# Kernel optimization log

Hardware: AMD Instinct MI355X
Metric: run time of the kernel (lower is better)

The kernel has to match this reference:

```python
import jax, jax.numpy as jnp
import numpy as np

B, T, NE, NH, HD = 4, 1024, 768, 12, 64
CURV = 0.0
EPS = 1e-6
LN_EPS = 1e-5
ROPE_BASE = 10000.0


def project(x, k):
    # Lift Euclidean vector onto Lorentz hyperboloid with curvature K = exp(k):
    # time coord t = sqrt(K + ||x||^2) so that <lx, lx>_L = -K.
    K = jnp.exp(k)
    t = jnp.sqrt(K + jnp.sum(x * x, axis=-1, keepdims=True))
    return jnp.concatenate([t, x], axis=-1)


def lorentz_distance(lq, lk, k):
    # lq, lk: (B, H, T, D+1); k: (1, H, 1, 1) log-curvature.
    # d = sqrt(K) * arccosh(clamp(-<q,k>_L / K, 1+eps))
    K = jnp.exp(k)
    inner = (jnp.einsum('bhid,bhjd->bhij', lq[..., 1:], lk[..., 1:])
             - jnp.einsum('bhi,bhj->bhij', lq[..., 0], lk[..., 0]))
    c = jnp.clip(-inner / K, 1.0 + EPS, None)
    return jnp.sqrt(K) * jnp.arccosh(c)


def lorentz_norm(x):
    # sqrt(|<x,x>_L|) with <x,x>_L = -x0^2 + ||xs||^2  (keepdim)
    inner = -x[..., 0:1] ** 2 + jnp.sum(x[..., 1:] ** 2, axis=-1, keepdims=True)
    return jnp.sqrt(jnp.clip(-inner, EPS, None))


def rotary_tables():
    inv_freq = 1.0 / (ROPE_BASE ** (np.arange(0, HD, 2, dtype=np.float32) / HD))
    t = np.arange(T, dtype=np.float32)
    freqs = np.outer(t, inv_freq)  # (T, HD/2)
    cos = jnp.asarray(np.cos(freqs))[None, :, None, :]  # (1,T,1,HD/2)
    sin = jnp.asarray(np.sin(freqs))[None, :, None, :]
    return cos, sin


def apply_rotary(x, cos, sin):
    # x: (B, T, H, HD)
    x1, x2 = x[..., : HD // 2], x[..., HD // 2:]
    return jnp.concatenate([x1 * cos + x2 * sin, -x1 * sin + x2 * cos], axis=-1)


def layernorm(y, g, b):
    m = jnp.mean(y, axis=-1, keepdims=True)
    v = jnp.mean((y - m) ** 2, axis=-1, keepdims=True)
    return (y - m) / jnp.sqrt(v + LN_EPS) * g + b


def setup_inputs() -> dict:
    key = jax.random.key(0)
    ks = jax.random.split(key, 8)
    s = 0.02
    return {
        'x': jax.random.normal(ks[0], (B, T, NE), dtype=jnp.float32),
        'block_curvature': jnp.asarray(CURV, dtype=jnp.float32),
        'mlp_curvature': jnp.asarray(CURV, dtype=jnp.float32),
        'attn_curvatures': jnp.ones((1, NH, 1, 1), dtype=jnp.float32) * CURV,
        'qkv_w': jax.random.normal(ks[1], (3 * NE, NE + 1), dtype=jnp.float32) * s,
        'attn_proj_w': jax.random.normal(ks[2], (NE, (HD + 1) * NH), dtype=jnp.float32) * s,
        'attn_proj_b': jnp.zeros((NE,), dtype=jnp.float32),
        'mlp_expand_w': jax.random.normal(ks[3], (4 * NE + 3, NE + 1), dtype=jnp.float32) * s,
        'mlp_expand_b': jnp.zeros((4 * NE + 3,), dtype=jnp.float32),
        'mlp_shrink_w': jax.random.normal(ks[4], (NE, 4 * (NE + 1)), dtype=jnp.float32) * s,
        'mlp_shrink_b': jnp.zeros((NE,), dtype=jnp.float32),
        'ln_g': jnp.ones((NE,), dtype=jnp.float32),
        'ln_b': jnp.zeros((NE,), dtype=jnp.float32),
    }


def reference(x, block_curvature, mlp_curvature, attn_curvatures, qkv_w,
              attn_proj_w, attn_proj_b, mlp_expand_w, mlp_expand_b,
              mlp_shrink_w, mlp_shrink_b, ln_g, ln_b):
    cos, sin = rotary_tables()
    causal_bias = jnp.where(
        jnp.triu(jnp.ones((T, T), dtype=bool), k=1), -jnp.inf, 0.0).astype(jnp.float32)

    def block_norm(lx):
        return project(layernorm(lx[..., 1:], ln_g, ln_b), block_curvature)

    def attn(lx):
        qkv = lx @ qkv_w.T  # (B, T, 3*NE)
        q, k, v = jnp.split(qkv, 3, axis=-1)
        q = apply_rotary(q.reshape(B, T, NH, HD), cos, sin)
        k = apply_rotary(k.reshape(B, T, NH, HD), cos, sin)
        v = v.reshape(B, T, NH, HD)
        lq = project(q.transpose(0, 2, 1, 3), attn_curvatures)  # (B,H,T,HD+1)
        lk = project(k.transpose(0, 2, 1, 3), attn_curvatures)
        lv = project(v.transpose(0, 2, 1, 3), attn_curvatures)
        dis = lorentz_distance(lq, lk, attn_curvatures)  # (B,H,T,T)
        aw = jax.nn.softmax(-dis + causal_bias, axis=-1)
        a = jnp.einsum('bhij,bhjd->bhid', aw, lv)  # (B,H,T,HD+1)
        a = a * jnp.sqrt(jnp.exp(attn_curvatures)) / lorentz_norm(a)
        a = a.transpose(0, 2, 1, 3).reshape(B, T, NH * (HD + 1))
        a = a @ attn_proj_w.T + attn_proj_b
        return project(a, block_curvature)

    def mlp(lx):
        h = lx @ mlp_expand_w.T + mlp_expand_b  # (B,T,4*NE+3)
        h = project(h, mlp_curvature)[..., 1:]  # drop time coord back to 4*NE+3
        h = jax.nn.gelu(h, approximate=False)
        h = project(h, mlp_curvature)  # (B,T,4*(NE+1))
        h = h @ mlp_shrink_w.T + mlp_shrink_b
        return project(h, block_curvature)

    def skip(lx, f_lx):
        return project(lx[..., 1:] + f_lx[..., 1:], block_curvature)

    lx = project(x, block_curvature)  # (B,T,NE+1)
    lx = skip(lx, attn(block_norm(lx)))
    lx = skip(lx, mlp(block_norm(lx)))
    return lx
```

## Files before the change

### kernel.cpp

```cpp
#include <hip/hip_runtime.h>
#include <cmath>

typedef unsigned short ushort_t;
typedef __attribute__((ext_vector_type(8))) short short8;
typedef __attribute__((ext_vector_type(4))) float floatx4;

#define NH    12
#define T     1024
#define ROWS  4096
#define NE    768
#define KPA   800
#define KPB   3104
#define NEXP  3200
#define HEXP  3075

__device__ __forceinline__ ushort_t f2bf(float f) {
  union { float f; unsigned u; } v; v.f = f;
  unsigned r = v.u + 0x7fffu + ((v.u >> 16) & 1u);
  return (ushort_t)(r >> 16);
}
__device__ __forceinline__ float bf2f(ushort_t b) {
  union { unsigned u; float f; } v; v.u = ((unsigned)b) << 16;
  return v.f;
}
__device__ __forceinline__ float blk_reduce_sum(float v, float* sm) {
  #pragma unroll
  for (int o = 32; o > 0; o >>= 1) v += __shfl_xor(v, o, 64);
  int lane = threadIdx.x & 63, w = threadIdx.x >> 6;
  __syncthreads();
  if (lane == 0) sm[w] = v;
  __syncthreads();
  return sm[0] + sm[1] + sm[2] + sm[3];
}
__device__ __forceinline__ float red16_sum(float v) {
  #pragma unroll
  for (int o = 1; o < 16; o <<= 1) v += __shfl_xor(v, o, 64);
  return v;
}
__device__ __forceinline__ float red16_max(float v) {
  #pragma unroll
  for (int o = 1; o < 16; o <<= 1) v = fmaxf(v, __shfl_xor(v, o, 64));
  return v;
}

__global__ void cvt_pad(ushort_t* __restrict__ dst, const float* __restrict__ src,
                        int rows, int srcK, int dstK, int rowsPad) {
  int idx = blockIdx.x * 256 + threadIdx.x;
  int total = rowsPad * dstK;
  if (idx >= total) return;
  int r = idx / dstK, c = idx - r * dstK;
  dst[idx] = (r < rows && c < srcK) ? f2bf(src[(size_t)r * srcK + c]) : (ushort_t)0;
}

__global__ void zero_aout_pad_bf(ushort_t* __restrict__ a) {
  int r = blockIdx.x * 256 + threadIdx.x;
  if (r < ROWS) {
    ushort_t* p = a + (size_t)r * KPA + 780;
    #pragma unroll
    for (int j = 0; j < 20; ++j) p[j] = 0;
  }
}

__global__ __launch_bounds__(256) void ln_project(
    const float* __restrict__ xin, const float* __restrict__ g,
    const float* __restrict__ bb, const float* __restrict__ curv,
    ushort_t* __restrict__ outp) {
  __shared__ float sm[4];
  const int row = blockIdx.x;
  const int tid = threadIdx.x;
  const float* xr = xin + (size_t)row * NE;
  float xv[3];
  float s = 0.f, ss = 0.f;
  #pragma unroll
  for (int i = 0; i < 3; ++i) {
    xv[i] = xr[tid + 256 * i];
    s += xv[i]; ss += xv[i] * xv[i];
  }
  s = blk_reduce_sum(s, sm);
  ss = blk_reduce_sum(ss, sm);
  float mean = s * (1.f / 768.f);
  float var = ss * (1.f / 768.f) - mean * mean;
  float rstd = rsqrtf(var + 1e-5f);
  float yv[3]; float ys = 0.f;
  #pragma unroll
  for (int i = 0; i < 3; ++i) {
    int c = tid + 256 * i;
    yv[i] = (xv[i] - mean) * rstd * g[c] + bb[c];
    ys += yv[i] * yv[i];
  }
  ys = blk_reduce_sum(ys, sm);
  float tc = sqrtf(expf(curv[0]) + ys);
  ushort_t* orow = outp + (size_t)row * KPA;
  #pragma unroll
  for (int i = 0; i < 3; ++i) orow[1 + tid + 256 * i] = f2bf(yv[i]);
  if (tid == 0) orow[0] = f2bf(tc);
  if (tid < KPA - 769) orow[769 + tid] = 0;
}

__global__ __launch_bounds__(256) void gemm_bf16(
    const ushort_t* __restrict__ A, int lda,
    const ushort_t* __restrict__ W, int ldw,
    void* __restrict__ Cout, int ldc,
    int nkTot, int cpt,
    const float* __restrict__ bias, int biasN,
    const float* __restrict__ res, int ldres,
    int outMode, float* __restrict__ Cp) {
  __shared__ ushort_t As[128 * 32];
  __shared__ ushort_t Bs[128 * 32];
  const int tid = threadIdx.x;
  const int w = tid >> 6, lane = tid & 63;
  const int rowBase = (int)blockIdx.y << 7;
  const int colBase = (int)blockIdx.x << 7;
  const int wm = (w & 1) * 64, wn = (w >> 1) * 64;
  const int lm = lane & 15, quad = lane >> 4;
  const int qp = quad ^ ((lm >> 1) & 3);

  floatx4 acc[4][4];
  #pragma unroll
  for (int i = 0; i < 4; ++i)
    #pragma unroll
    for (int j = 0; j < 4; ++j) {
      floatx4 z = {0.f, 0.f, 0.f, 0.f};
      acc[i][j] = z;
    }

  const int kt0 = (int)blockIdx.z * cpt;
  const int kt1 = min(nkTot, kt0 + cpt);
  for (int kt = kt0; kt < kt1; ++kt) {
    __syncthreads();
    #pragma unroll
    for (int j = 0; j < 2; ++j) {
      int p = w * 128 + j * 64 + lane;
      int r = p >> 2;
      int gq = (p & 3) ^ ((r >> 1) & 3);
      const ushort_t* ga = A + (size_t)(rowBase + r) * lda + kt * 32 + gq * 8;
      const ushort_t* gb = W + (size_t)(colBase + r) * ldw + kt * 32 + gq * 8;
      __builtin_amdgcn_global_load_lds(
          (const __attribute__((address_space(1))) void*)ga,
          (__attribute__((address_space(3))) void*)&As[(w * 128 + j * 64) * 8],
          16, 0, 0);
      __builtin_amdgcn_global_load_lds(
          (const __attribute__((address_space(1))) void*)gb,
          (__attribute__((address_space(3))) void*)&Bs[(w * 128 + j * 64) * 8],
          16, 0, 0);
    }
    __syncthreads();

    short8 af[4], bfr[4];
    #pragma unroll
    for (int i = 0; i < 4; ++i) {
      af[i]  = *(const short8*)&As[(wm + i * 16 + lm) * 32 + qp * 8];
      bfr[i] = *(const short8*)&Bs[(wn + i * 16 + lm) * 32 + qp * 8];
    }
    #pragma unroll
    for (int i = 0; i < 4; ++i)
      #pragma unroll
      for (int jn = 0; jn < 4; ++jn)
        acc[i][jn] = __builtin_amdgcn_mfma_f32_16x16x32_bf16(
            af[i], bfr[jn], acc[i][jn], 0, 0, 0);
  }

  if (gridDim.z > 1) {
    float* dst = Cp + (size_t)blockIdx.z * ROWS * ldc;
    #pragma unroll
    for (int i = 0; i < 4; ++i)
      #pragma unroll
      for (int jn = 0; jn < 4; ++jn) {
        const int col = colBase + wn + jn * 16 + lm;
        #pragma unroll
        for (int rg = 0; rg < 4; ++rg) {
          const int row = rowBase + wm + i * 16 + quad * 4 + rg;
          dst[(size_t)row * ldc + col] = acc[i][jn][rg];
        }
      }
  } else if (outMode == 1) {
    ushort_t* C = (ushort_t*)Cout;
    #pragma unroll
    for (int i = 0; i < 4; ++i)
      #pragma unroll
      for (int jn = 0; jn < 4; ++jn) {
        const int col = colBase + wn + jn * 16 + lm;
        const float bv = bias ? ((col < biasN) ? bias[col] : 0.f) : 0.f;
        #pragma unroll
        for (int rg = 0; rg < 4; ++rg) {
          const int row = rowBase + wm + i * 16 + quad * 4 + rg;
          C[(size_t)row * ldc + col] = f2bf(acc[i][jn][rg] + bv);
        }
      }
  } else {
    float* C = (float*)Cout;
    #pragma unroll
    for (int i = 0; i < 4; ++i)
      #pragma unroll
      for (int jn = 0; jn < 4; ++jn) {
        const int col = colBase + wn + jn * 16 + lm;
        const float bv = bias ? ((col < biasN) ? bias[col] : 0.f) : 0.f;
        #pragma unroll
        for (int rg = 0; rg < 4; ++rg) {
          const int row = rowBase + wm + i * 16 + quad * 4 + rg;
          float o = acc[i][jn][rg] + bv;
          if (res) o += res[(size_t)row * ldres + col];
          C[(size_t)row * ldc + col] = o;
        }
      }
  }
}

__global__ __launch_bounds__(256) void reduce_split(
    const float* __restrict__ Cp, int nsplit,
    const float* __restrict__ bias, const float* __restrict__ res,
    float* __restrict__ outp) {
  int idx = blockIdx.x * 256 + threadIdx.x;
  const int n4 = ROWS * NE / 4;
  if (idx >= n4) return;
  float4 s = ((const float4*)Cp)[idx];
  for (int sp = 1; sp < nsplit; ++sp) {
    float4 t = ((const float4*)(Cp + (size_t)sp * ROWS * NE))[idx];
    s.x += t.x; s.y += t.y; s.z += t.z; s.w += t.w;
  }
  float4 bv = *(const float4*)&bias[(idx * 4) % NE];
  float4 rv = ((const float4*)res)[idx];
  s.x += bv.x + rv.x; s.y += bv.y + rv.y;
  s.z += bv.z + rv.z; s.w += bv.w + rv.w;
  ((float4*)outp)[idx] = s;
}

__global__ __launch_bounds__(256) void rope_project(
    const float* __restrict__ qkv, const float* __restrict__ ac,
    ushort_t* __restrict__ qb, ushort_t* __restrict__ kb, ushort_t* __restrict__ vtb,
    float* __restrict__ q0, float* __restrict__ k0, float* __restrict__ v0) {
  int gid = blockIdx.x * 4 + (threadIdx.x >> 6);
  int lane = threadIdx.x & 63;
  int h = gid % NH;
  int bt = gid / NH;
  int t = bt & (T - 1);
  int b = bt >> 10;
  size_t base = (size_t)bt * 2304 + h * 64;
  float qv = qkv[base + lane];
  float kv = qkv[base + 768 + lane];
  float vv = qkv[base + 1536 + lane];
  int f = lane & 31;
  float ang = (float)t * powf(10000.f, -(float)f * (1.f / 32.f));
  float sn, cs;
  sincosf(ang, &sn, &cs);
  float qp = __shfl(qv, lane ^ 32, 64);
  float kp = __shfl(kv, lane ^ 32, 64);
  float qr = (lane < 32) ? (qv * cs + qp * sn) : (-qp * sn + qv * cs);
  float kr = (lane < 32) ? (kv * cs + kp * sn) : (-kp * sn + kv * cs);
  float Kh = expf(ac[h]);
  float sq = qr * qr, sk = kr * kr, sv = vv * vv;
  #pragma unroll
  for (int o = 32; o > 0; o >>= 1) {
    sq += __shfl_xor(sq, o, 64);
    sk += __shfl_xor(sk, o, 64);
    sv += __shfl_xor(sv, o, 64);
  }
  size_t idx = ((size_t)(b * NH + h) * T + t);
  qb[idx * 64 + lane] = f2bf(qr);
  kb[idx * 64 + lane] = f2bf(kr);
  vtb[(size_t)(b * NH + h) * (64 * T) + (size_t)lane * T + t] = f2bf(vv);
  if (lane == 0) {
    q0[idx] = sqrtf(Kh + sq);
    k0[idx] = sqrtf(Kh + sk);
    v0[idx] = sqrtf(Kh + sv);
  }
}

__global__ __launch_bounds__(256) void attn_kernel(
    const ushort_t* __restrict__ qb, const ushort_t* __restrict__ kb,
    const ushort_t* __restrict__ vtb,
    const float* __restrict__ q0, const float* __restrict__ k0,
    const float* __restrict__ v0,
    const float* __restrict__ ac, ushort_t* __restrict__ aout) {
  __shared__ ushort_t Qs[64 * 64];
  __shared__ ushort_t Ks[64 * 64];
  __shared__ ushort_t Vts[64 * 64];
  __shared__ ushort_t Ps[64 * 72];

  const int bh = blockIdx.y;
  const int h = bh % NH;
  const int b = bh / NH;
  const int qtile = (int)gridDim.x - 1 - (int)blockIdx.x;
  const int qt0 = qtile * 64;
  const int tid = threadIdx.x;
  const int w = tid >> 6, lane = tid & 63;
  const int lm = lane & 15, quad = lane >> 4;
  const int wm = w * 16;
  const int sw = lm & 7;

  const float Kh = expf(ac[h]);
  const float sqrtK = sqrtf(Kh);
  const float invK = 1.0f / Kh;

  {
    const ushort_t* qt = qb + ((size_t)bh * T + qt0) * 64;
    #pragma unroll
    for (int j = 0; j < 2; ++j) {
      int e = (j * 4 + w) * 512 + lane * 8;
      int r = e >> 6, chs = (e >> 3) & 7;
      int clog = (chs ^ (r & 7)) * 8;
      __builtin_amdgcn_global_load_lds(
          (const __attribute__((address_space(1))) void*)(qt + r * 64 + clog),
          (__attribute__((address_space(3))) void*)&Qs[(j * 4 + w) * 512],
          16, 0, 0);
    }
  }
  float q0rv[4];
  #pragma unroll
  for (int r = 0; r < 4; ++r)
    q0rv[r] = q0[(size_t)bh * T + qt0 + wm + quad * 4 + r];

  float mrow[4], lsum[4], a0r[4];
  floatx4 oacc[4];
  #pragma unroll
  for (int r = 0; r < 4; ++r) { mrow[r] = -__builtin_inff(); lsum[r] = 0.f; a0r[r] = 0.f; }
  #pragma unroll
  for (int nt = 0; nt < 4; ++nt) { floatx4 z = {0.f,0.f,0.f,0.f}; oacc[nt] = z; }

  const int ntiles = qtile + 1;
  for (int kt = 0; kt < ntiles; ++kt) {
    const int j0 = kt * 64;
    __syncthreads();
    {
      const ushort_t* ktile = kb + ((size_t)bh * T + j0) * 64;
      const ushort_t* vbh = vtb + (size_t)bh * (64 * T);
      #pragma unroll
      for (int j = 0; j < 2; ++j) {
        int e = (j * 4 + w) * 512 + lane * 8;
        int r = e >> 6, chs = (e >> 3) & 7;
        int clog = (chs ^ (r & 7)) * 8;
        __builtin_amdgcn_global_load_lds(
            (const __attribute__((address_space(1))) void*)(ktile + r * 64 + clog),
            (__attribute__((address_space(3))) void*)&Ks[(j * 4 + w) * 512],
            16, 0, 0);
        __builtin_amdgcn_global_load_lds(
            (const __attribute__((address_space(1))) void*)(vbh + (size_t)r * T + j0 + clog),
            (__attribute__((address_space(3))) void*)&Vts[(j * 4 + w) * 512],
            16, 0, 0);
      }
    }
    float k0v[4], v0v[4];
    #pragma unroll
    for (int jt = 0; jt < 4; ++jt) {
      k0v[jt] = k0[(size_t)bh * T + j0 + jt * 16 + lm];
      v0v[jt] = v0[(size_t)bh * T + j0 + jt * 16 + lm];
    }
    __syncthreads();

    short8 qf0 = *(const short8*)&Qs[(wm + lm) * 64 + ((0 + quad) ^ sw) * 8];
    short8 qf1 = *(const short8*)&Qs[(wm + lm) * 64 + ((4 + quad) ^ sw) * 8];
    floatx4 sacc[4];
    #pragma unroll
    for (int jt = 0; jt < 4; ++jt) {
      const int krow = jt * 16 + lm;
      short8 kf0 = *(const short8*)&Ks[krow * 64 + ((0 + quad) ^ sw) * 8];
      short8 kf1 = *(const short8*)&Ks[krow * 64 + ((4 + quad) ^ sw) * 8];
      floatx4 z = {0.f, 0.f, 0.f, 0.f};
      z = __builtin_amdgcn_mfma_f32_16x16x32_bf16(qf0, kf0, z, 0, 0, 0);
      z = __builtin_amdgcn_mfma_f32_16x16x32_bf16(qf1, kf1, z, 0, 0, 0);
      sacc[jt] = z;
    }

    const bool diag = (kt == qtile);
    float alpha[4];
    #pragma unroll
    for (int r = 0; r < 4; ++r) {
      const int i = qt0 + wm + quad * 4 + r;
      float sc[4];
      float rowm = -__builtin_inff();
      #pragma unroll
      for (int jt = 0; jt < 4; ++jt) {
        float c = (q0rv[r] * k0v[jt] - sacc[jt][r]) * invK;
        float u = fmaxf(c - 1.f, 1e-6f);
        float s = -sqrtK * __logf(1.f + u + sqrtf(u * (u + 2.f)));
        if (diag && (j0 + jt * 16 + lm > i)) s = -__builtin_inff();
        sc[jt] = s;
        rowm = fmaxf(rowm, s);
      }
      rowm = red16_max(rowm);
      const float mnew = fmaxf(mrow[r], rowm);
      alpha[r] = __expf(mrow[r] - mnew);
      mrow[r] = mnew;
      float ls = 0.f, a0s = 0.f;
      #pragma unroll
      for (int jt = 0; jt < 4; ++jt) {
        float p = __expf(sc[jt] - mnew);
        ushort_t pb = f2bf(p);
        Ps[(wm + quad * 4 + r) * 72 + jt * 16 + lm] = pb;
        float pf = bf2f(pb);
        ls += pf;
        a0s += pf * v0v[jt];
      }
      lsum[r] = lsum[r] * alpha[r] + ls;
      a0r[r]  = a0r[r]  * alpha[r] + a0s;
    }

    #pragma unroll
    for (int nt = 0; nt < 4; ++nt)
      #pragma unroll
      for (int r = 0; r < 4; ++r) oacc[nt][r] *= alpha[r];
    short8 pf0 = *(const short8*)&Ps[(wm + lm) * 72 + quad * 8];
    short8 pf1 = *(const short8*)&Ps[(wm + lm) * 72 + 32 + quad * 8];
    #pragma unroll
    for (int nt = 0; nt < 4; ++nt) {
      const int vrow = nt * 16 + lm;
      short8 vf0 = *(const short8*)&Vts[vrow * 64 + ((0 + quad) ^ sw) * 8];
      short8 vf1 = *(const short8*)&Vts[vrow * 64 + ((4 + quad) ^ sw) * 8];
      oacc[nt] = __builtin_amdgcn_mfma_f32_16x16x32_bf16(pf0, vf0, oacc[nt], 0, 0, 0);
      oacc[nt] = __builtin_amdgcn_mfma_f32_16x16x32_bf16(pf1, vf1, oacc[nt], 0, 0, 0);
    }
  }

  #pragma unroll
  for (int r = 0; r < 4; ++r) {
    float lf = red16_sum(lsum[r]);
    float a0f = red16_sum(a0r[r]);
    const float invl = 1.f / lf;
    float av[4]; float ssq = 0.f;
    #pragma unroll
    for (int nt = 0; nt < 4; ++nt) { av[nt] = oacc[nt][r] * invl; ssq += av[nt] * av[nt]; }
    ssq = red16_sum(ssq);
    const float a0n = a0f * invl;
    const float nsq = fmaxf(a0n * a0n - ssq, 1e-6f);
    const float scale = sqrtK * rsqrtf(nsq);
    const int i = qt0 + wm + quad * 4 + r;
    ushort_t* orow = aout + (size_t)(b * T + i) * KPA + h * 65;
    #pragma unroll
    for (int nt = 0; nt < 4; ++nt) orow[1 + nt * 16 + lm] = f2bf(av[nt] * scale);
    if (lm == 0) orow[0] = f2bf(a0n * scale);
  }
}

__global__ __launch_bounds__(256) void gelu_project(
    const ushort_t* __restrict__ hsrc, const float* __restrict__ curv,
    ushort_t* __restrict__ hp) {
  __shared__ float sm[4];
  const int row = blockIdx.x;
  const int tid = threadIdx.x;
  const ushort_t* hr = hsrc + (size_t)row * NEXP;
  float gv[13];
  float ss = 0.f;
  #pragma unroll
  for (int i = 0; i < 13; ++i) {
    int c = tid + 256 * i;
    float xx = (c < HEXP) ? bf2f(hr[c]) : 0.f;
    float gg = 0.5f * xx * (1.f + erff(xx * 0.70710678118654752f));
    gv[i] = gg; ss += gg * gg;
  }
  ss = blk_reduce_sum(ss, sm);
  float tc = sqrtf(expf(curv[0]) + ss);
  ushort_t* orow = hp + (size_t)row * KPB;
  #pragma unroll
  for (int i = 0; i < 13; ++i) {
    int c = tid + 256 * i;
    if (c < HEXP) orow[1 + c] = f2bf(gv[i]);
  }
  if (tid == 0) orow[0] = f2bf(tc);
  if (tid < KPB - (HEXP + 1)) orow[HEXP + 1 + tid] = 0;
}

__global__ __launch_bounds__(256) void final_project(
    const float* __restrict__ x3, const float* __restrict__ curv, float* __restrict__ out) {
  __shared__ float sm[4];
  const int row = blockIdx.x;
  const int tid = threadIdx.x;
  const float* xr = x3 + (size_t)row * NE;
  float v[3]; float ss = 0.f;
  #pragma unroll
  for (int i = 0; i < 3; ++i) { v[i] = xr[tid + 256 * i]; ss += v[i] * v[i]; }
  ss = blk_reduce_sum(ss, sm);
  float tc = sqrtf(expf(curv[0]) + ss);
  float* o = out + (size_t)row * 769;
  #pragma unroll
  for (int i = 0; i < 3; ++i) o[1 + tid + 256 * i] = v[i];
  if (tid == 0) o[0] = tc;
}

extern "C" void kernel_launch(void* const* d_in, const int* in_sizes, int n_in,
                              void* d_out, int out_size, void* d_ws, size_t ws_size,
                              hipStream_t stream) {
  (void)in_sizes; (void)n_in; (void)out_size; (void)ws_size;
  const float* x     = (const float*)d_in[0];
  const float* bc    = (const float*)d_in[1];
  const float* mc    = (const float*)d_in[2];
  const float* ac    = (const float*)d_in[3];
  const float* qkvw  = (const float*)d_in[4];
  const float* projw = (const float*)d_in[5];
  const float* projb = (const float*)d_in[6];
  const float* expw  = (const float*)d_in[7];
  const float* expb  = (const float*)d_in[8];
  const float* shrw  = (const float*)d_in[9];
  const float* shrb  = (const float*)d_in[10];
  const float* lng   = (const float*)d_in[11];
  const float* lnb   = (const float*)d_in[12];
  float* out = (float*)d_out;

  float* x2 = (float*)d_ws;
  ushort_t* qkv_wb  = (ushort_t*)(x2 + (size_t)ROWS * NE);
  ushort_t* proj_wb = qkv_wb + (size_t)2304 * KPA;
  ushort_t* exp_wb  = proj_wb + (size_t)768 * KPA;
  ushort_t* shr_wb  = exp_wb + (size_t)NEXP * KPA;
  ushort_t* lnp_bf  = shr_wb + (size_t)768 * KPB;
  ushort_t* aout_bf = lnp_bf + (size_t)ROWS * KPA;
  char* r2 = (char*)(aout_bf + (size_t)ROWS * KPA);
  float* qkvb = (float*)r2;
  ushort_t* qbb = (ushort_t*)(qkvb + (size_t)ROWS * 2304);
  ushort_t* kbb = qbb + (size_t)48 * T * 64;
  ushort_t* vtb = kbb + (size_t)48 * T * 64;
  float* q0b = (float*)(vtb + (size_t)48 * T * 64);
  float* k0b = q0b + (size_t)48 * T;
  float* v0b = k0b + (size_t)48 * T;
  float* ppartP = (float*)r2;
  ushort_t* hbbf = (ushort_t*)r2;
  ushort_t* hp_bf = hbbf + (size_t)ROWS * NEXP;
  float* ppartS = (float*)(hp_bf + (size_t)ROWS * KPB);

  cvt_pad<<<(2304 * KPA + 255) / 256, 256, 0, stream>>>(qkv_wb, qkvw, 2304, 769, KPA, 2304);
  cvt_pad<<<(768 * KPA + 255) / 256, 256, 0, stream>>>(proj_wb, projw, 768, 780, KPA, 768);
  cvt_pad<<<(NEXP * KPA + 255) / 256, 256, 0, stream>>>(exp_wb, expw, HEXP, 769, KPA, NEXP);
  cvt_pad<<<(768 * KPB + 255) / 256, 256, 0, stream>>>(shr_wb, shrw, 768, 3076, KPB, 768);
  zero_aout_pad_bf<<<(ROWS + 255) / 256, 256, 0, stream>>>(aout_bf);

  ln_project<<<ROWS, 256, 0, stream>>>(x, lng, lnb, bc, lnp_bf);
  gemm_bf16<<<dim3(2304 / 128, ROWS / 128, 1), 256, 0, stream>>>(
      lnp_bf, KPA, qkv_wb, KPA, qkvb, 2304, KPA / 32, KPA / 32,
      nullptr, 0, nullptr, 0, 0, nullptr);
  rope_project<<<(ROWS * NH) / 4, 256, 0, stream>>>(qkvb, ac, qbb, kbb, vtb, q0b, k0b, v0b);
  attn_kernel<<<dim3(T / 64, 48), 256, 0, stream>>>(qbb, kbb, vtb, q0b, k0b, v0b, ac, aout_bf);
  gemm_bf16<<<dim3(768 / 128, ROWS / 128, 2), 256, 0, stream>>>(
      aout_bf, KPA, proj_wb, KPA, nullptr, NE, KPA / 32, 13,
      nullptr, 0, nullptr, 0, 0, ppartP);
  reduce_split<<<(ROWS * NE / 4 + 255) / 256, 256, 0, stream>>>(
      ppartP, 2, projb, x, x2);
  ln_project<<<ROWS, 256, 0, stream>>>(x2, lng, lnb, bc, lnp_bf);
  gemm_bf16<<<dim3(NEXP / 128, ROWS / 128, 1), 256, 0, stream>>>(
      lnp_bf, KPA, exp_wb, KPA, hbbf, NEXP, KPA / 32, KPA / 32,
      expb, HEXP, nullptr, 0, 1, nullptr);
  gelu_project<<<ROWS, 256, 0, stream>>>(hbbf, mc, hp_bf);
  gemm_bf16<<<dim3(768 / 128, ROWS / 128, 4), 256, 0, stream>>>(
      hp_bf, KPB, shr_wb, KPB, nullptr, NE, KPB / 32, 25,
      nullptr, 0, nullptr, 0, 0, ppartS);
  reduce_split<<<(ROWS * NE / 4 + 255) / 256, 256, 0, stream>>>(
      ppartS, 4, shrb, x2, x2);
  final_project<<<ROWS, 256, 0, stream>>>(x2, bc, out);
}
```

Before: 432.9 us.

## Split attention over KV halves, fuse reductions with layernorm, merge prep kernels

Attention is split into two KV-range halves per query tile, with partial O/m/l/a0 written to workspace and merged in a new combine kernel. This gives a more even spread of causal work across blocks. The split-K reduce is fused with the following layernorm/projection and with the final projection, and the four weight conversions plus pad zeroing are merged into one prep launch. The cost is extra partial-result traffic and one more launch for the combine step.

```diff
diff --git a/kernel.cpp b/kernel.cpp
--- a/kernel.cpp
+++ b/kernel.cpp
@@ -13,6 +13,7 @@
 #define KPB   3104
 #define NEXP  3200
 #define HEXP  3075
+#define NSPLIT 2
 
 __device__ __forceinline__ ushort_t f2bf(float f) {
   union { float f; unsigned u; } v; v.f = f;
@@ -43,19 +44,36 @@
   return v;
 }
 
-__global__ void cvt_pad(ushort_t* __restrict__ dst, const float* __restrict__ src,
-                        int rows, int srcK, int dstK, int rowsPad) {
-  int idx = blockIdx.x * 256 + threadIdx.x;
-  int total = rowsPad * dstK;
-  if (idx >= total) return;
+#define NB_A 7200
+#define NB_B 2400
+#define NB_C 10000
+#define NB_D 9312
+#define NB_E 16
+__device__ __forceinline__ void cvt_elem(ushort_t* __restrict__ dst,
+                                         const float* __restrict__ src,
+                                         int idx, int srcRows, int srcK, int dstK) {
   int r = idx / dstK, c = idx - r * dstK;
-  dst[idx] = (r < rows && c < srcK) ? f2bf(src[(size_t)r * srcK + c]) : (ushort_t)0;
-}
-
-__global__ void zero_aout_pad_bf(ushort_t* __restrict__ a) {
-  int r = blockIdx.x * 256 + threadIdx.x;
-  if (r < ROWS) {
-    ushort_t* p = a + (size_t)r * KPA + 780;
+  dst[idx] = (r < srcRows && c < srcK) ? f2bf(src[(size_t)r * srcK + c]) : (ushort_t)0;
+}
+__global__ __launch_bounds__(256) void prep_kernel(
+    ushort_t* __restrict__ qkv_wb, const float* __restrict__ qkvw,
+    ushort_t* __restrict__ proj_wb, const float* __restrict__ projw,
+    ushort_t* __restrict__ exp_wb, const float* __restrict__ expw,
+    ushort_t* __restrict__ shr_wb, const float* __restrict__ shrw,
+    ushort_t* __restrict__ aout_bf) {
+  int blk = blockIdx.x;
+  int tid = threadIdx.x;
+  if (blk < NB_A) {
+    cvt_elem(qkv_wb, qkvw, blk * 256 + tid, 2304, 769, KPA);
+  } else if (blk < NB_A + NB_B) {
+    cvt_elem(proj_wb, projw, (blk - NB_A) * 256 + tid, 768, 780, KPA);
+  } else if (blk < NB_A + NB_B + NB_C) {
+    cvt_elem(exp_wb, expw, (blk - NB_A - NB_B) * 256 + tid, HEXP, 769, KPA);
+  } else if (blk < NB_A + NB_B + NB_C + NB_D) {
+    cvt_elem(shr_wb, shrw, (blk - NB_A - NB_B - NB_C) * 256 + tid, 768, 3076, KPB);
+  } else {
+    int r = (blk - NB_A - NB_B - NB_C - NB_D) * 256 + tid;
+    ushort_t* p = aout_bf + (size_t)r * KPA + 780;
     #pragma unroll
     for (int j = 0; j < 20; ++j) p[j] = 0;
   }
@@ -204,25 +222,6 @@
         }
       }
   }
-}
-
-__global__ __launch_bounds__(256) void reduce_split(
-    const float* __restrict__ Cp, int nsplit,
-    const float* __restrict__ bias, const float* __restrict__ res,
-    float* __restrict__ outp) {
-  int idx = blockIdx.x * 256 + threadIdx.x;
-  const int n4 = ROWS * NE / 4;
-  if (idx >= n4) return;
-  float4 s = ((const float4*)Cp)[idx];
-  for (int sp = 1; sp < nsplit; ++sp) {
-    float4 t = ((const float4*)(Cp + (size_t)sp * ROWS * NE))[idx];
-    s.x += t.x; s.y += t.y; s.z += t.z; s.w += t.w;
-  }
-  float4 bv = *(const float4*)&bias[(idx * 4) % NE];
-  float4 rv = ((const float4*)res)[idx];
-  s.x += bv.x + rv.x; s.y += bv.y + rv.y;
-  s.z += bv.z + rv.z; s.w += bv.w + rv.w;
-  ((float4*)outp)[idx] = s;
 }
 
 __global__ __launch_bounds__(256) void rope_project(
@@ -271,22 +270,42 @@
     const ushort_t* __restrict__ vtb,
     const float* __restrict__ q0, const float* __restrict__ k0,
     const float* __restrict__ v0,
-    const float* __restrict__ ac, ushort_t* __restrict__ aout) {
+    const float* __restrict__ ac,
+    float* __restrict__ Opart, float* __restrict__ mpart,
+    float* __restrict__ lpart, float* __restrict__ a0part) {
   __shared__ ushort_t Qs[64 * 64];
   __shared__ ushort_t Ks[64 * 64];
   __shared__ ushort_t Vts[64 * 64];
   __shared__ ushort_t Ps[64 * 72];
 
-  const int bh = blockIdx.y;
+  const int sIdx = blockIdx.x;
+  const int qtile = (int)gridDim.y - 1 - (int)blockIdx.y;
+  const int bh = blockIdx.z;
   const int h = bh % NH;
-  const int b = bh / NH;
-  const int qtile = (int)gridDim.x - 1 - (int)blockIdx.x;
   const int qt0 = qtile * 64;
   const int tid = threadIdx.x;
   const int w = tid >> 6, lane = tid & 63;
   const int lm = lane & 15, quad = lane >> 4;
   const int wm = w * 16;
   const int sw = lm & 7;
+
+  const int n = qtile + 1;
+  const int half = (n + 1) >> 1;
+  const int kbeg = sIdx ? half : 0;
+  const int kend = sIdx ? n : half;
+  const size_t pb = (size_t)(sIdx * 48 + bh) * T;
+
+  if (kbeg >= kend) {
+    #pragma unroll
+    for (int r = 0; r < 4; ++r) {
+      const int i = qt0 + wm + quad * 4 + r;
+      float* orow = Opart + (pb + i) * 64;
+      #pragma unroll
+      for (int nt = 0; nt < 4; ++nt) orow[nt * 16 + lm] = 0.f;
+      if (lm == 0) { mpart[pb + i] = -1e30f; lpart[pb + i] = 0.f; a0part[pb + i] = 0.f; }
+    }
+    return;
+  }
 
   const float Kh = expf(ac[h]);
   const float sqrtK = sqrtf(Kh);
@@ -317,8 +336,7 @@
   #pragma unroll
   for (int nt = 0; nt < 4; ++nt) { floatx4 z = {0.f,0.f,0.f,0.f}; oacc[nt] = z; }
 
-  const int ntiles = qtile + 1;
-  for (int kt = 0; kt < ntiles; ++kt) {
+  for (int kt = kbeg; kt < kend; ++kt) {
     const int j0 = kt * 64;
     __syncthreads();
     {
@@ -385,9 +403,9 @@
       #pragma unroll
       for (int jt = 0; jt < 4; ++jt) {
         float p = __expf(sc[jt] - mnew);
-        ushort_t pb = f2bf(p);
-        Ps[(wm + quad * 4 + r) * 72 + jt * 16 + lm] = pb;
-        float pf = bf2f(pb);
+        ushort_t pb2 = f2bf(p);
+        Ps[(wm + quad * 4 + r) * 72 + jt * 16 + lm] = pb2;
+        float pf = bf2f(pb2);
         ls += pf;
         a0s += pf * v0v[jt];
       }
@@ -415,20 +433,43 @@
   for (int r = 0; r < 4; ++r) {
     float lf = red16_sum(lsum[r]);
     float a0f = red16_sum(a0r[r]);
-    const float invl = 1.f / lf;
-    float av[4]; float ssq = 0.f;
-    #pragma unroll
-    for (int nt = 0; nt < 4; ++nt) { av[nt] = oacc[nt][r] * invl; ssq += av[nt] * av[nt]; }
-    ssq = red16_sum(ssq);
-    const float a0n = a0f * invl;
-    const float nsq = fmaxf(a0n * a0n - ssq, 1e-6f);
-    const float scale = sqrtK * rsqrtf(nsq);
     const int i = qt0 + wm + quad * 4 + r;
-    ushort_t* orow = aout + (size_t)(b * T + i) * KPA + h * 65;
-    #pragma unroll
-    for (int nt = 0; nt < 4; ++nt) orow[1 + nt * 16 + lm] = f2bf(av[nt] * scale);
-    if (lm == 0) orow[0] = f2bf(a0n * scale);
-  }
+    float* orow = Opart + (pb + i) * 64;
+    #pragma unroll
+    for (int nt = 0; nt < 4; ++nt) orow[nt * 16 + lm] = oacc[nt][r];
+    if (lm == 0) { mpart[pb + i] = mrow[r]; lpart[pb + i] = lf; a0part[pb + i] = a0f; }
+  }
+}
+
+__global__ __launch_bounds__(256) void attn_combine(
+    const float* __restrict__ Opart, const float* __restrict__ mpart,
+    const float* __restrict__ lpart, const float* __restrict__ a0part,
+    const float* __restrict__ ac, ushort_t* __restrict__ aout) {
+  const int widx = blockIdx.x * 4 + (threadIdx.x >> 6);
+  const int lane = threadIdx.x & 63;
+  const int bh = widx >> 10;
+  const int t = widx & 1023;
+  const int h = bh % NH, b = bh / NH;
+  const size_t r0 = (size_t)bh * T + t;
+  const size_t r1 = (size_t)(48 + bh) * T + t;
+  float m0 = mpart[r0], m1 = mpart[r1];
+  float M = fmaxf(m0, m1);
+  float w0 = __expf(m0 - M), w1 = __expf(m1 - M);
+  float L = w0 * lpart[r0] + w1 * lpart[r1];
+  float A0 = w0 * a0part[r0] + w1 * a0part[r1];
+  float O = w0 * Opart[r0 * 64 + lane] + w1 * Opart[r1 * 64 + lane];
+  const float invl = 1.f / L;
+  float av = O * invl;
+  float ssq = av * av;
+  #pragma unroll
+  for (int o = 32; o > 0; o >>= 1) ssq += __shfl_xor(ssq, o, 64);
+  float a0n = A0 * invl;
+  float nsq = fmaxf(a0n * a0n - ssq, 1e-6f);
+  float Kh = expf(ac[h]);
+  float scale = sqrtf(Kh) * rsqrtf(nsq);
+  ushort_t* orow = aout + (size_t)(b * T + t) * KPA + h * 65;
+  orow[1 + lane] = f2bf(av * scale);
+  if (lane == 0) orow[0] = f2bf(a0n * scale);
 }
 
 __global__ __launch_bounds__(256) void gelu_project(
@@ -459,15 +500,64 @@
   if (tid < KPB - (HEXP + 1)) orow[HEXP + 1 + tid] = 0;
 }
 
-__global__ __launch_bounds__(256) void final_project(
-    const float* __restrict__ x3, const float* __restrict__ curv, float* __restrict__ out) {
+__global__ __launch_bounds__(256) void reduce_ln_project(
+    const float* __restrict__ Cp, int nsplit,
+    const float* __restrict__ bias, const float* __restrict__ res,
+    float* __restrict__ x2out,
+    const float* __restrict__ g, const float* __restrict__ bb,
+    const float* __restrict__ curv, ushort_t* __restrict__ lnp) {
   __shared__ float sm[4];
   const int row = blockIdx.x;
   const int tid = threadIdx.x;
-  const float* xr = x3 + (size_t)row * NE;
+  float xv[3];
+  float s = 0.f, ss = 0.f;
+  #pragma unroll
+  for (int i = 0; i < 3; ++i) {
+    const int c = tid + 256 * i;
+    float v = bias[c] + res[(size_t)row * NE + c];
+    for (int sp = 0; sp < nsplit; ++sp)
+      v += Cp[(size_t)sp * ROWS * NE + (size_t)row * NE + c];
+    x2out[(size_t)row * NE + c] = v;
+    xv[i] = v;
+    s += v; ss += v * v;
+  }
+  s = blk_reduce_sum(s, sm);
+  ss = blk_reduce_sum(ss, sm);
+  float mean = s * (1.f / 768.f);
+  float var = ss * (1.f / 768.f) - mean * mean;
+  float rstd = rsqrtf(var + 1e-5f);
+  float yv[3]; float ys = 0.f;
+  #pragma unroll
+  for (int i = 0; i < 3; ++i) {
+    int c = tid + 256 * i;
+    yv[i] = (xv[i] - mean) * rstd * g[c] + bb[c];
+    ys += yv[i] * yv[i];
+  }
+  ys = blk_reduce_sum(ys, sm);
+  float tc = sqrtf(expf(curv[0]) + ys);
+  ushort_t* orow = lnp + (size_t)row * KPA;
+  #pragma unroll
+  for (int i = 0; i < 3; ++i) orow[1 + tid + 256 * i] = f2bf(yv[i]);
+  if (tid == 0) orow[0] = f2bf(tc);
+  if (tid < KPA - 769) orow[769 + tid] = 0;
+}
+
+__global__ __launch_bounds__(256) void reduce_final_project(
+    const float* __restrict__ Cp, int nsplit,
+    const float* __restrict__ bias, const float* __restrict__ res,
+    const float* __restrict__ curv, float* __restrict__ out) {
+  __shared__ float sm[4];
+  const int row = blockIdx.x;
+  const int tid = threadIdx.x;
   float v[3]; float ss = 0.f;
   #pragma unroll
-  for (int i = 0; i < 3; ++i) { v[i] = xr[tid + 256 * i]; ss += v[i] * v[i]; }
+  for (int i = 0; i < 3; ++i) {
+    const int c = tid + 256 * i;
+    float t = bias[c] + res[(size_t)row * NE + c];
+    for (int sp = 0; sp < nsplit; ++sp)
+      t += Cp[(size_t)sp * ROWS * NE + (size_t)row * NE + c];
+    v[i] = t; ss += t * t;
+  }
   ss = blk_reduce_sum(ss, sm);
   float tc = sqrtf(expf(curv[0]) + ss);
   float* o = out + (size_t)row * 769;
@@ -510,29 +600,30 @@
   float* q0b = (float*)(vtb + (size_t)48 * T * 64);
   float* k0b = q0b + (size_t)48 * T;
   float* v0b = k0b + (size_t)48 * T;
+  float* Opart = v0b + (size_t)48 * T;
+  float* mpart = Opart + (size_t)NSPLIT * 48 * T * 64;
+  float* lpart = mpart + (size_t)NSPLIT * 48 * T;
+  float* a0part = lpart + (size_t)NSPLIT * 48 * T;
   float* ppartP = (float*)r2;
   ushort_t* hbbf = (ushort_t*)r2;
   ushort_t* hp_bf = hbbf + (size_t)ROWS * NEXP;
   float* ppartS = (float*)(hp_bf + (size_t)ROWS * KPB);
 
-  cvt_pad<<<(2304 * KPA + 255) / 256, 256, 0, stream>>>(qkv_wb, qkvw, 2304, 769, KPA, 2304);
-  cvt_pad<<<(768 * KPA + 255) / 256, 256, 0, stream>>>(proj_wb, projw, 768, 780, KPA, 768);
-  cvt_pad<<<(NEXP * KPA + 255) / 256, 256, 0, stream>>>(exp_wb, expw, HEXP, 769, KPA, NEXP);
-  cvt_pad<<<(768 * KPB + 255) / 256, 256, 0, stream>>>(shr_wb, shrw, 768, 3076, KPB, 768);
-  zero_aout_pad_bf<<<(ROWS + 255) / 256, 256, 0, stream>>>(aout_bf);
-
+  prep_kernel<<<NB_A + NB_B + NB_C + NB_D + NB_E, 256, 0, stream>>>(
+      qkv_wb, qkvw, proj_wb, projw, exp_wb, expw, shr_wb, shrw, aout_bf);
   ln_project<<<ROWS, 256, 0, stream>>>(x, lng, lnb, bc, lnp_bf);
   gemm_bf16<<<dim3(2304 / 128, ROWS / 128, 1), 256, 0, stream>>>(
       lnp_bf, KPA, qkv_wb, KPA, qkvb, 2304, KPA / 32, KPA / 32,
       nullptr, 0, nullptr, 0, 0, nullptr);
   rope_project<<<(ROWS * NH) / 4, 256, 0, stream>>>(qkvb, ac, qbb, kbb, vtb, q0b, k0b, v0b);
-  attn_kernel<<<dim3(T / 64, 48), 256, 0, stream>>>(qbb, kbb, vtb, q0b, k0b, v0b, ac, aout_bf);
+  attn_kernel<<<dim3(NSPLIT, T / 64, 48), 256, 0, stream>>>(
+      qbb, kbb, vtb, q0b, k0b, v0b, ac, Opart, mpart, lpart, a0part);
+  attn_combine<<<(48 * T) / 4, 256, 0, stream>>>(Opart, mpart, lpart, a0part, ac, aout_bf);
   gemm_bf16<<<dim3(768 / 128, ROWS / 128, 2), 256, 0, stream>>>(
       aout_bf, KPA, proj_wb, KPA, nullptr, NE, KPA / 32, 13,
       nullptr, 0, nullptr, 0, 0, ppartP);
-  reduce_split<<<(ROWS * NE / 4 + 255) / 256, 256, 0, stream>>>(
-      ppartP, 2, projb, x, x2);
-  ln_project<<<ROWS, 256, 0, stream>>>(x2, lng, lnb, bc, lnp_bf);
+  reduce_ln_project<<<ROWS, 256, 0, stream>>>(
+      ppartP, 2, projb, x, x2, lng, lnb, bc, lnp_bf);
   gemm_bf16<<<dim3(NEXP / 128, ROWS / 128, 1), 256, 0, stream>>>(
       lnp_bf, KPA, exp_wb, KPA, hbbf, NEXP, KPA / 32, KPA / 32,
       expb, HEXP, nullptr, 0, 1, nullptr);
@@ -540,7 +631,6 @@
   gemm_bf16<<<dim3(768 / 128, ROWS / 128, 4), 256, 0, stream>>>(
       hp_bf, KPB, shr_wb, KPB, nullptr, NE, KPB / 32, 25,
       nullptr, 0, nullptr, 0, 0, ppartS);
-  reduce_split<<<(ROWS * NE / 4 + 255) / 256, 256, 0, stream>>>(
-      ppartS, 4, shrb, x2, x2);
-  final_project<<<ROWS, 256, 0, stream>>>(x2, bc, out);
-}
+  reduce_final_project<<<ROWS, 256, 0, stream>>>(
+      ppartS, 4, shrb, x2, bc, out);
+}
```

Result: no change. 436.2 us (+0.8%).
